# Performance work log

Hardware: AMD Instinct MI355X
Metric: run time of the kernel (lower is better)

## Reference

```python
import jax, jax.numpy as jnp
import numpy as np

B, S, D, A_DIM = 8, 2048, 256, 64

def setup_inputs() -> dict:
    key = jax.random.key(0)
    k_x, k_wm, k_wl, k_eps = jax.random.split(key, 4)
    return {
        "x": jax.random.normal(k_x, (B, S, D), dtype=jnp.float32),
        "W_mean": jax.random.normal(k_wm, (D, A_DIM), dtype=jnp.float32) * (1.0 / np.sqrt(D)),
        "b_mean": jnp.zeros((A_DIM,), dtype=jnp.float32),
        "W_logvar": jax.random.normal(k_wl, (D, A_DIM), dtype=jnp.float32) * (1.0 / np.sqrt(D)),
        "b_logvar": jnp.zeros((A_DIM,), dtype=jnp.float32),
        "eps": jax.random.normal(k_eps, (B, S, A_DIM), dtype=jnp.float32),
    }

def reference(x, W_mean, b_mean, W_logvar, b_logvar, eps):
    d = x.shape[-1]
    scale = 1.0 / jnp.sqrt(jnp.asarray(d, dtype=x.dtype))
    # S_det = x x^T / sqrt(d)  -> [B, S, S]
    scores = jnp.einsum("bsd,btd->bst", x, x) * scale
    attn = jax.nn.softmax(scores, axis=-1)
    # A_det = softmax(S) x  -> [B, S, D]
    A_det = jnp.einsum("bst,btd->bsd", attn, x)
    A_mean = A_det @ W_mean + b_mean        # [B, S, A_DIM]
    A_logvar = A_det @ W_logvar + b_logvar  # [B, S, A_DIM]
    A = A_mean + jnp.exp(0.5 * A_logvar) * eps  # sqrt(exp(logvar)) = exp(logvar/2)
    return (A_mean, A_logvar, A)
```

## Files before the change

kernel.cpp:

```cpp
#include <hip/hip_runtime.h>

#define B_ 8
#define S_ 2048
#define D_ 256

typedef _Float16 f16;
typedef f16 f16x2 __attribute__((ext_vector_type(2)));
typedef f16 f16x8 __attribute__((ext_vector_type(8)));
typedef float f32x16 __attribute__((ext_vector_type(16)));
typedef unsigned int u32;
typedef u32 u32x4 __attribute__((ext_vector_type(4)));

typedef const __attribute__((address_space(1))) unsigned int* gptr_t;
typedef __attribute__((address_space(3))) unsigned int* lptr_t;

__device__ __forceinline__ void gload_lds16(const void* g, void* l) {
  __builtin_amdgcn_global_load_lds((gptr_t)(unsigned long long)g,
                                   (lptr_t)(unsigned long long)l, 16, 0, 0);
}

__device__ __forceinline__ u32 packf16(float a, float b) {
  f16x2 t; t[0] = (f16)a; t[1] = (f16)b;
  return __builtin_bit_cast(u32, t);
}

__device__ __forceinline__ void barrier_raw() {
  __builtin_amdgcn_sched_barrier(0);
  __builtin_amdgcn_s_barrier();
  __builtin_amdgcn_sched_barrier(0);
}

__device__ __forceinline__ void pack16(const f32x16& p, int hi, u32x4& o0, u32x4& o1) {
#pragma unroll
  for (int c2 = 0; c2 < 2; ++c2) {
    u32 a1 = packf16(p[8 * c2 + 0], p[8 * c2 + 1]);
    u32 a2 = packf16(p[8 * c2 + 2], p[8 * c2 + 3]);
    u32 b1 = packf16(p[8 * c2 + 4], p[8 * c2 + 5]);
    u32 b2 = packf16(p[8 * c2 + 6], p[8 * c2 + 7]);
    u32 xa1 = __shfl_xor(a1, 32), xa2 = __shfl_xor(a2, 32);
    u32 xb1 = __shfl_xor(b1, 32), xb2 = __shfl_xor(b2, 32);
    u32x4 f;
    f[0] = hi ? xb1 : a1;
    f[1] = hi ? xb2 : a2;
    f[2] = hi ? b1 : xa1;
    f[3] = hi ? b2 : xa2;
    if (c2) o1 = f; else o0 = f;
  }
}

#define SC2F 0.09016844f
#define NMAXR 20.0f
#define SWZ(r, s) ((s) ^ ((r) & 3) ^ (((r) >> 2) & 3))

__global__ void prep(const float* __restrict__ x, const float* __restrict__ Wm,
                     const float* __restrict__ Wl, f16* __restrict__ xh,
                     f16* __restrict__ xt, float* __restrict__ n2,
                     f16* __restrict__ Wt) {
  __shared__ f16 tile[64][264];
  const int bid = blockIdx.x;
  const int t = threadIdx.x;
  if (bid < 256) {
    const int b = bid >> 5, st = bid & 31;
    const int s0 = st * 64;
    const float* xb = x + ((size_t)(b * S_ + s0)) * D_;
    f16* xhb = xh + ((size_t)(b * S_ + s0)) * D_;
#pragma unroll
    for (int it = 0; it < 16; ++it) {
      int flat = it * 256 + t;
      int r = flat >> 6, c4 = flat & 63;
      float4 v = *reinterpret_cast<const float4*>(xb + r * 256 + c4 * 4);
      f16 h0 = (f16)v.x, h1 = (f16)v.y, h2 = (f16)v.z, h3 = (f16)v.w;
      f16x2 p0 = {h0, h1}, p1 = {h2, h3};
      uint2 wv; wv.x = __builtin_bit_cast(u32, p0); wv.y = __builtin_bit_cast(u32, p1);
      *reinterpret_cast<uint2*>(xhb + r * 256 + c4 * 4) = wv;
      tile[r][c4 * 4 + 0] = h0; tile[r][c4 * 4 + 1] = h1;
      tile[r][c4 * 4 + 2] = h2; tile[r][c4 * 4 + 3] = h3;
    }
    __syncthreads();
    {
      int r = t >> 2, qd = t & 3;
      float s = 0.0f;
#pragma unroll
      for (int i = 0; i < 8; ++i) {
        f16x8 v = *reinterpret_cast<const f16x8*>(&tile[r][qd * 64 + i * 8]);
#pragma unroll
        for (int u = 0; u < 8; ++u) { float f = (float)v[u]; s += f * f; }
      }
      s += __shfl_xor(s, 1); s += __shfl_xor(s, 2);
      if (qd == 0) n2[b * S_ + s0 + r] = s;
    }
    {
      f16* xtb = xt + ((size_t)(b * D_ + t)) * S_ + s0;
#pragma unroll
      for (int s8 = 0; s8 < 8; ++s8) {
        f16x8 ov;
#pragma unroll
        for (int u = 0; u < 8; ++u) ov[u] = tile[s8 * 8 + u][t];
        *reinterpret_cast<f16x8*>(xtb + s8 * 8) = ov;
      }
    }
  } else {
    int idx = (bid - 256) * 1024 + t * 4;
    int j = idx >> 8, d = idx & 255;
#pragma unroll
    for (int k2 = 0; k2 < 4; ++k2) {
      float v = (j < 64) ? Wm[(d + k2) * 64 + j] : Wl[(d + k2) * 64 + (j - 64)];
      Wt[idx + k2] = (f16)v;
    }
  }
}

__launch_bounds__(512, 4)
__global__ void gemm1_kern(const f16* __restrict__ xh, const float* __restrict__ n2,
                           f16* __restrict__ P, float* __restrict__ Lp,
                           int b0, int bm, int bsh) {
  __shared__ f16 Aq[2][4096];
  __shared__ f16 Bk[2][8192];
  const int idx = blockIdx.x;
  const int bl = idx & bm;
  const int kt = (idx >> bsh) & 7;
  const int qt = idx >> (bsh + 3);
  const int b = b0 + bl;
  const int qb = qt * 128, kb = kt * 256;
  const int tid = threadIdx.x, lane = tid & 63, w = tid >> 6;
  const int l31 = lane & 31, hi = lane >> 5;
  const int wq = w >> 2, wk = w & 3;
  const f16* xb = xh + (size_t)b * S_ * D_;

#define G1_STAGE(st, pp)                                                       \
  {                                                                            \
    { int c = tid; int r = c >> 2, sl = c & 3; int cs = SWZ(r, sl);            \
      gload_lds16(xb + (size_t)(qb + r) * 256 + (st) * 32 + cs * 8,            \
                  &Aq[pp][0] + c * 8); }                                       \
    _Pragma("unroll") for (int i = 0; i < 2; ++i) {                            \
      int c = i * 512 + tid; int r = c >> 2, sl = c & 3; int cs = SWZ(r, sl);  \
      gload_lds16(xb + (size_t)(kb + r) * 256 + (st) * 32 + cs * 8,            \
                  &Bk[pp][0] + c * 8); }                                       \
  }

#define G1_COMP(pp)                                                           \
  { _Pragma("unroll") for (int kc = 0; kc < 2; ++kc) {                        \
      int s = kc * 2 + hi;                                                    \
      f16x8 af[2], bf[2];                                                     \
      _Pragma("unroll") for (int mi = 0; mi < 2; ++mi) {                      \
        int row = wk * 64 + mi * 32 + l31;                                    \
        af[mi] = *reinterpret_cast<const f16x8*>(&Bk[pp][row * 32 + SWZ(row, s) * 8]); } \
      _Pragma("unroll") for (int ni = 0; ni < 2; ++ni) {                      \
        int row = wq * 64 + ni * 32 + l31;                                    \
        bf[ni] = *reinterpret_cast<const f16x8*>(&Aq[pp][row * 32 + SWZ(row, s) * 8]); } \
      _Pragma("unroll") for (int mi = 0; mi < 2; ++mi)                        \
        _Pragma("unroll") for (int ni = 0; ni < 2; ++ni)                      \
          acc[mi][ni] = __builtin_amdgcn_mfma_f32_32x32x16_f16(af[mi], bf[ni], acc[mi][ni], 0, 0, 0); \
    } }

  f32x16 acc[2][2];
#pragma unroll
  for (int i = 0; i < 2; ++i)
#pragma unroll
    for (int j = 0; j < 2; ++j)
#pragma unroll
      for (int e = 0; e < 16; ++e) acc[i][j][e] = 0.0f;

  G1_STAGE(0, 0);
  __syncthreads();
#pragma unroll 1
  for (int t = 0; t < 8; ++t) {
    const int p = t & 1;
    if (t < 7) G1_STAGE(t + 1, p ^ 1);
    G1_COMP(p);
    __syncthreads();
  }
#undef G1_STAGE
#undef G1_COMP

  float r2[2], lsum[2];
  int qrow[2];
#pragma unroll
  for (int ni = 0; ni < 2; ++ni) {
    qrow[ni] = qb + wq * 64 + ni * 32 + l31;
    r2[ni] = sqrtf(n2[b * S_ + qrow[ni]]) * (NMAXR * SC2F);
    lsum[ni] = 0.0f;
  }
#pragma unroll
  for (int mi = 0; mi < 2; ++mi)
#pragma unroll
    for (int ni = 0; ni < 2; ++ni)
#pragma unroll
      for (int j = 0; j < 16; ++j) {
        float v = exp2f(acc[mi][ni][j] * SC2F - r2[ni]);
        acc[mi][ni][j] = v;
        lsum[ni] += v;
      }
#pragma unroll
  for (int ni = 0; ni < 2; ++ni) lsum[ni] += __shfl_xor(lsum[ni], 32);

#pragma unroll
  for (int mi = 0; mi < 2; ++mi)
#pragma unroll
    for (int ni = 0; ni < 2; ++ni) {
      u32x4 s0, s1;
      pack16(acc[mi][ni], hi, s0, s1);
      size_t rowp = (size_t)(bl * S_ + qrow[ni]) * 2048;
      int colb = kb + wk * 64 + mi * 32;
      *reinterpret_cast<u32x4*>(P + rowp + colb + hi * 8) = s0;
      *reinterpret_cast<u32x4*>(P + rowp + colb + 16 + hi * 8) = s1;
    }

  float* Lred = (float*)(&Aq[0][0]);
  if (hi == 0) {
    Lred[(wq * 64 + l31) * 4 + wk] = lsum[0];
    Lred[(wq * 64 + 32 + l31) * 4 + wk] = lsum[1];
  }
  __syncthreads();
  if (tid < 128) {
    float s = Lred[tid * 4] + Lred[tid * 4 + 1] + Lred[tid * 4 + 2] + Lred[tid * 4 + 3];
    Lp[(size_t)(bl * 8 + kt) * 2048 + qb + tid] = s;
  }
}

__launch_bounds__(256, 3)
__global__ void gemm2_kern(const f16* __restrict__ P, const f16* __restrict__ xt,
                           const float* __restrict__ Lp, f16* __restrict__ adet,
                           int b0, int bm, int bsh) {
  __shared__ f16 Pt[4][2048];
  __shared__ f16 Xt[4][4096];
  const int idx = blockIdx.x;
  const int bl = idx & bm;
  const int dt = (idx >> bsh) & 1;
  const int qt = idx >> (bsh + 1);
  const int b = b0 + bl;
  const int qb = qt * 64, db = dt * 128;
  const int tid = threadIdx.x, lane = tid & 63, w = tid >> 6;
  const int l31 = lane & 31, hi = lane >> 5;
  const int wq = w & 1, wd = w >> 1;
  const f16* xtb = xt + (size_t)b * D_ * S_;

#define G2_STAGE(tt, tb)                                                       \
  {                                                                            \
    { int c = tid; int r = c >> 2, sl = c & 3; int cs = SWZ(r, sl);            \
      gload_lds16(P + (size_t)(bl * S_ + qb + r) * 2048 + (tt) * 32 + cs * 8,  \
                  &Pt[tb][0] + c * 8); }                                       \
    _Pragma("unroll") for (int i = 0; i < 2; ++i) {                            \
      int c = i * 256 + tid; int r = c >> 2, sl = c & 3; int cs = SWZ(r, sl);  \
      gload_lds16(xtb + (size_t)(db + r) * 2048 + (tt) * 32 + cs * 8,          \
                  &Xt[tb][0] + c * 8); }                                       \
  }

#define G2_COMP(tb)                                                           \
  { _Pragma("unroll") for (int kc = 0; kc < 2; ++kc) {                        \
      int s = kc * 2 + hi;                                                    \
      int qrow = wq * 32 + l31;                                               \
      f16x8 bf = *reinterpret_cast<const f16x8*>(&Pt[tb][qrow * 32 + SWZ(qrow, s) * 8]); \
      _Pragma("unroll") for (int ni = 0; ni < 2; ++ni) {                      \
        int drow = wd * 64 + ni * 32 + l31;                                   \
        f16x8 af = *reinterpret_cast<const f16x8*>(&Xt[tb][drow * 32 + SWZ(drow, s) * 8]); \
        acc[ni] = __builtin_amdgcn_mfma_f32_32x32x16_f16(af, bf, acc[ni], 0, 0, 0); \
      } } }

  f32x16 acc[2];
#pragma unroll
  for (int i = 0; i < 2; ++i)
#pragma unroll
    for (int e = 0; e < 16; ++e) acc[i][e] = 0.0f;

  G2_STAGE(0, 0);
  G2_STAGE(1, 1);
  G2_STAGE(2, 2);
#pragma unroll 1
  for (int t = 0; t < 62; ++t) {
    asm volatile("s_waitcnt vmcnt(6)" ::: "memory");
    barrier_raw();
    if (t < 61) G2_STAGE(t + 3, (t + 3) & 3);
    G2_COMP(t & 3);
  }
  asm volatile("s_waitcnt vmcnt(3)" ::: "memory");
  barrier_raw();
  G2_COMP(2);
  asm volatile("s_waitcnt vmcnt(0)" ::: "memory");
  barrier_raw();
  G2_COMP(3);
#undef G2_STAGE
#undef G2_COMP

  const int q = qb + wq * 32 + l31;
  float L = 0.0f;
#pragma unroll
  for (int kt = 0; kt < 8; ++kt) L += Lp[(size_t)(bl * 8 + kt) * 2048 + q];
  float rL = 1.0f / L;
#pragma unroll
  for (int ni = 0; ni < 2; ++ni)
#pragma unroll
    for (int e = 0; e < 16; ++e) acc[ni][e] *= rL;
#pragma unroll
  for (int ni = 0; ni < 2; ++ni) {
    u32x4 s0, s1;
    pack16(acc[ni], hi, s0, s1);
    f16* arow = adet + (size_t)(b * S_ + q) * 256 + db + wd * 64 + ni * 32;
    *reinterpret_cast<u32x4*>(arow + hi * 8) = s0;
    *reinterpret_cast<u32x4*>(arow + 16 + hi * 8) = s1;
  }
}

__launch_bounds__(64)
__global__ void proj_kern(const f16* __restrict__ adet, const f16* __restrict__ Wt,
                          const float* __restrict__ bm, const float* __restrict__ bl,
                          const float* __restrict__ eps, float* __restrict__ out) {
  const int lane = threadIdx.x & 63;
  const int l31 = lane & 31, hi = lane >> 5;
  const int bidx = blockIdx.x;
  const int rb = ((bidx & 7) * 64 + (bidx >> 3)) * 32;
  f16x8 af[16];
  const f16* arow = adet + (size_t)(rb + l31) * 256;
#pragma unroll
  for (int kk = 0; kk < 16; ++kk)
    af[kk] = *reinterpret_cast<const f16x8*>(arow + kk * 16 + hi * 8);
  f32x16 acc[4];
#pragma unroll
  for (int i = 0; i < 4; ++i)
#pragma unroll
    for (int j = 0; j < 16; ++j) acc[i][j] = 0.0f;
#pragma unroll
  for (int ns = 0; ns < 4; ++ns) {
    const f16* wrow = Wt + (size_t)(l31 + 32 * ns) * 256;
#pragma unroll
    for (int kk = 0; kk < 16; ++kk) {
      f16x8 bf = *reinterpret_cast<const f16x8*>(wrow + kk * 16 + hi * 8);
      acc[ns] = __builtin_amdgcn_mfma_f32_32x32x16_f16(af[kk], bf, acc[ns], 0, 0, 0);
    }
  }
#pragma unroll
  for (int ns = 0; ns < 2; ++ns) {
    int c = l31 + 32 * ns;
    float bmv = bm[c], blv = bl[c];
#pragma unroll
    for (int r = 0; r < 16; ++r) {
      int row = (r & 3) + 8 * (r >> 2) + 4 * hi;
      int grow = rb + row;
      float mean = acc[ns][r] + bmv;
      float lv = acc[ns + 2][r] + blv;
      float e = eps[grow * 64 + c];
      float a = mean + exp2f(0.7213475204f * lv) * e;
      out[grow * 64 + c] = mean;
      out[1048576 + grow * 64 + c] = lv;
      out[2097152 + grow * 64 + c] = a;
    }
  }
}

extern "C" void kernel_launch(void* const* d_in, const int* in_sizes, int n_in,
                              void* d_out, int out_size, void* d_ws, size_t ws_size,
                              hipStream_t stream) {
  (void)in_sizes; (void)n_in; (void)out_size;
  const float* x   = (const float*)d_in[0];
  const float* Wm  = (const float*)d_in[1];
  const float* bmv = (const float*)d_in[2];
  const float* Wl  = (const float*)d_in[3];
  const float* blv = (const float*)d_in[4];
  const float* ep  = (const float*)d_in[5];
  float* out = (float*)d_out;

  char* ws = (char*)d_ws;
  f16*   xh   = (f16*)(ws + 0);
  f16*   xt   = (f16*)(ws + 8388608);
  f16*   adet = (f16*)(ws + 16777216);
  f16*   Wt   = (f16*)(ws + 25165824);
  float* n2   = (float*)(ws + 25231360);
  float* Lp   = (float*)(ws + 25296896);
  const size_t P_off = 25821184;
  f16*   Pbuf = (f16*)(ws + P_off);

  int bpp = 1;
  if      (ws_size >= P_off + (size_t)8 * 2048 * 2048 * 2) bpp = 8;
  else if (ws_size >= P_off + (size_t)4 * 2048 * 2048 * 2) bpp = 4;
  else if (ws_size >= P_off + (size_t)2 * 2048 * 2048 * 2) bpp = 2;
  const int bsh = (bpp == 8) ? 3 : (bpp == 4) ? 2 : (bpp == 2) ? 1 : 0;
  const int bm = bpp - 1;

  prep<<<288, 256, 0, stream>>>(x, Wm, Wl, xh, xt, n2, Wt);
  for (int b0 = 0; b0 < 8; b0 += bpp) {
    gemm1_kern<<<bpp * 128, 512, 0, stream>>>(xh, n2, Pbuf, Lp, b0, bm, bsh);
    gemm2_kern<<<bpp * 64, 256, 0, stream>>>(Pbuf, xt, Lp, adet, b0, bm, bsh);
  }
  proj_kern<<<512, 64, 0, stream>>>(adet, Wt, bmv, blv, ep, out);
}
```

Measured before the change: 89.81 us.

## Exploit score symmetry: compute upper-triangle tiles and mirror-write transposed P

Because scores = x x^T is symmetric, gemm1 now computes only the upper-triangular 128x128 tiles (136 per batch instead of the full grid) and writes both the tile and its transpose to P. The transposed tile is staged through shared memory with an XOR swizzle and exponentiated using the key-row norm bound. The row-sum partials buffer Lp is removed, and gemm2 instead accumulates the softmax denominator from the f16 P fragments it already loads. This halves the score GEMM FLOPs at the cost of an extra LDS transpose pass, a larger LDS footprint, and denominator sums taken from f16-rounded values.

```diff
diff --git a/kernel.cpp b/kernel.cpp
--- a/kernel.cpp
+++ b/kernel.cpp
@@ -112,116 +112,126 @@
 
 __launch_bounds__(512, 4)
 __global__ void gemm1_kern(const f16* __restrict__ xh, const float* __restrict__ n2,
-                           f16* __restrict__ P, float* __restrict__ Lp,
-                           int b0, int bm, int bsh) {
-  __shared__ f16 Aq[2][4096];
-  __shared__ f16 Bk[2][8192];
+                           f16* __restrict__ P, int b0, int bm, int bsh) {
+  __shared__ __align__(16) char smem[65536];
+  f16* Aq = (f16*)smem;
+  f16* Bk = (f16*)(smem + 32768);
   const int idx = blockIdx.x;
   const int bl = idx & bm;
-  const int kt = (idx >> bsh) & 7;
-  const int qt = idx >> (bsh + 3);
+  int tdec = idx >> bsh;
+  int qt = 0;
+#pragma unroll 1
+  while (tdec >= 16 - qt) { tdec -= 16 - qt; ++qt; }
+  const int kt = qt + tdec;
   const int b = b0 + bl;
-  const int qb = qt * 128, kb = kt * 256;
+  const int qb = qt * 128, kb = kt * 128;
   const int tid = threadIdx.x, lane = tid & 63, w = tid >> 6;
   const int l31 = lane & 31, hi = lane >> 5;
   const int wq = w >> 2, wk = w & 3;
   const f16* xb = xh + (size_t)b * S_ * D_;
 
 #define G1_STAGE(st, pp)                                                       \
-  {                                                                            \
-    { int c = tid; int r = c >> 2, sl = c & 3; int cs = SWZ(r, sl);            \
-      gload_lds16(xb + (size_t)(qb + r) * 256 + (st) * 32 + cs * 8,            \
-                  &Aq[pp][0] + c * 8); }                                       \
-    _Pragma("unroll") for (int i = 0; i < 2; ++i) {                            \
-      int c = i * 512 + tid; int r = c >> 2, sl = c & 3; int cs = SWZ(r, sl);  \
-      gload_lds16(xb + (size_t)(kb + r) * 256 + (st) * 32 + cs * 8,            \
-                  &Bk[pp][0] + c * 8); }                                       \
-  }
-
-#define G1_COMP(pp)                                                           \
-  { _Pragma("unroll") for (int kc = 0; kc < 2; ++kc) {                        \
-      int s = kc * 2 + hi;                                                    \
-      f16x8 af[2], bf[2];                                                     \
-      _Pragma("unroll") for (int mi = 0; mi < 2; ++mi) {                      \
-        int row = wk * 64 + mi * 32 + l31;                                    \
-        af[mi] = *reinterpret_cast<const f16x8*>(&Bk[pp][row * 32 + SWZ(row, s) * 8]); } \
-      _Pragma("unroll") for (int ni = 0; ni < 2; ++ni) {                      \
-        int row = wq * 64 + ni * 32 + l31;                                    \
-        bf[ni] = *reinterpret_cast<const f16x8*>(&Aq[pp][row * 32 + SWZ(row, s) * 8]); } \
-      _Pragma("unroll") for (int mi = 0; mi < 2; ++mi)                        \
-        _Pragma("unroll") for (int ni = 0; ni < 2; ++ni)                      \
-          acc[mi][ni] = __builtin_amdgcn_mfma_f32_32x32x16_f16(af[mi], bf[ni], acc[mi][ni], 0, 0, 0); \
+  { _Pragma("unroll") for (int i = 0; i < 4; ++i) {                            \
+      int ii = w * 4 + i;                                                      \
+      int flat = ii * 64 + lane;                                               \
+      bool isB = ii >= 16;                                                     \
+      int ch = isB ? flat - 1024 : flat;                                       \
+      int r = ch >> 3, c = ch & 7;                                             \
+      int csrc = c ^ (r & 7);                                                  \
+      const f16* src = xb + (size_t)((isB ? kb : qb) + r) * 256 +              \
+                       (st) * 64 + csrc * 8;                                   \
+      f16* dst = (isB ? Bk : Aq) + ((pp) * 8192) + ch * 8;                     \
+      gload_lds16(src, dst);                                                   \
     } }
 
-  f32x16 acc[2][2];
+  f32x16 acc[2];
 #pragma unroll
   for (int i = 0; i < 2; ++i)
 #pragma unroll
-    for (int j = 0; j < 2; ++j)
-#pragma unroll
-      for (int e = 0; e < 16; ++e) acc[i][j][e] = 0.0f;
+    for (int e = 0; e < 16; ++e) acc[i][e] = 0.0f;
 
   G1_STAGE(0, 0);
   __syncthreads();
-#pragma unroll 1
-  for (int t = 0; t < 8; ++t) {
+#pragma unroll
+  for (int t = 0; t < 4; ++t) {
     const int p = t & 1;
-    if (t < 7) G1_STAGE(t + 1, p ^ 1);
-    G1_COMP(p);
+    if (t < 3) G1_STAGE(t + 1, p ^ 1);
+#pragma unroll
+    for (int kc = 0; kc < 4; ++kc) {
+      int cc = ((2 * kc + hi) ^ (l31 & 7)) * 8;
+      f16x8 af  = *reinterpret_cast<const f16x8*>(Bk + p * 8192 + (wk * 32 + l31) * 64 + cc);
+      f16x8 bf0 = *reinterpret_cast<const f16x8*>(Aq + p * 8192 + (wq * 64 + l31) * 64 + cc);
+      f16x8 bf1 = *reinterpret_cast<const f16x8*>(Aq + p * 8192 + (wq * 64 + 32 + l31) * 64 + cc);
+      acc[0] = __builtin_amdgcn_mfma_f32_32x32x16_f16(af, bf0, acc[0], 0, 0, 0);
+      acc[1] = __builtin_amdgcn_mfma_f32_32x32x16_f16(af, bf1, acc[1], 0, 0, 0);
+    }
     __syncthreads();
   }
 #undef G1_STAGE
-#undef G1_COMP
-
-  float r2[2], lsum[2];
+
+  float* raw = (float*)smem;
+  if (kt != qt) {
+#pragma unroll
+    for (int ni = 0; ni < 2; ++ni)
+#pragma unroll
+      for (int j = 0; j < 16; ++j) {
+        int kvloc = wk * 32 + (j & 3) + 8 * (j >> 2) + 4 * hi;
+        int qloc = wq * 64 + ni * 32 + l31;
+        raw[kvloc * 128 + (qloc ^ ((kvloc & 7) << 2))] = acc[ni][j];
+      }
+  }
+
+  float r2[2];
   int qrow[2];
 #pragma unroll
   for (int ni = 0; ni < 2; ++ni) {
     qrow[ni] = qb + wq * 64 + ni * 32 + l31;
     r2[ni] = sqrtf(n2[b * S_ + qrow[ni]]) * (NMAXR * SC2F);
-    lsum[ni] = 0.0f;
-  }
-#pragma unroll
-  for (int mi = 0; mi < 2; ++mi)
-#pragma unroll
-    for (int ni = 0; ni < 2; ++ni)
-#pragma unroll
-      for (int j = 0; j < 16; ++j) {
-        float v = exp2f(acc[mi][ni][j] * SC2F - r2[ni]);
-        acc[mi][ni][j] = v;
-        lsum[ni] += v;
-      }
-#pragma unroll
-  for (int ni = 0; ni < 2; ++ni) lsum[ni] += __shfl_xor(lsum[ni], 32);
-
-#pragma unroll
-  for (int mi = 0; mi < 2; ++mi)
-#pragma unroll
-    for (int ni = 0; ni < 2; ++ni) {
-      u32x4 s0, s1;
-      pack16(acc[mi][ni], hi, s0, s1);
-      size_t rowp = (size_t)(bl * S_ + qrow[ni]) * 2048;
-      int colb = kb + wk * 64 + mi * 32;
-      *reinterpret_cast<u32x4*>(P + rowp + colb + hi * 8) = s0;
-      *reinterpret_cast<u32x4*>(P + rowp + colb + 16 + hi * 8) = s1;
-    }
-
-  float* Lred = (float*)(&Aq[0][0]);
-  if (hi == 0) {
-    Lred[(wq * 64 + l31) * 4 + wk] = lsum[0];
-    Lred[(wq * 64 + 32 + l31) * 4 + wk] = lsum[1];
-  }
-  __syncthreads();
-  if (tid < 128) {
-    float s = Lred[tid * 4] + Lred[tid * 4 + 1] + Lred[tid * 4 + 2] + Lred[tid * 4 + 3];
-    Lp[(size_t)(bl * 8 + kt) * 2048 + qb + tid] = s;
+  }
+#pragma unroll
+  for (int ni = 0; ni < 2; ++ni)
+#pragma unroll
+    for (int j = 0; j < 16; ++j)
+      acc[ni][j] = exp2f(acc[ni][j] * SC2F - r2[ni]);
+
+  const int colb = kb + wk * 32;
+#pragma unroll
+  for (int ni = 0; ni < 2; ++ni) {
+    u32x4 s0, s1;
+    pack16(acc[ni], hi, s0, s1);
+    size_t rowp = (size_t)(bl * S_ + qrow[ni]) * 2048;
+    *reinterpret_cast<u32x4*>(P + rowp + colb + hi * 8) = s0;
+    *reinterpret_cast<u32x4*>(P + rowp + colb + 16 + hi * 8) = s1;
+  }
+
+  if (kt != qt) {
+    __syncthreads();
+    const int kvr = tid >> 2;
+    const int qseg = (tid & 3) * 32;
+    float r2kv = sqrtf(n2[b * S_ + kb + kvr]) * (NMAXR * SC2F);
+    u32 ow[16];
+#pragma unroll
+    for (int c8 = 0; c8 < 8; ++c8) {
+      int qs = qseg + c8 * 4;
+      float4 v = *reinterpret_cast<const float4*>(
+          &raw[kvr * 128 + (qs ^ ((kvr & 7) << 2))]);
+      ow[c8 * 2 + 0] = packf16(exp2f(v.x * SC2F - r2kv), exp2f(v.y * SC2F - r2kv));
+      ow[c8 * 2 + 1] = packf16(exp2f(v.z * SC2F - r2kv), exp2f(v.w * SC2F - r2kv));
+    }
+    size_t rowp = (size_t)(bl * S_ + kb + kvr) * 2048;
+#pragma unroll
+    for (int sseg = 0; sseg < 4; ++sseg) {
+      u32x4 sv;
+      sv[0] = ow[sseg * 4 + 0]; sv[1] = ow[sseg * 4 + 1];
+      sv[2] = ow[sseg * 4 + 2]; sv[3] = ow[sseg * 4 + 3];
+      *reinterpret_cast<u32x4*>(P + rowp + qb + qseg + sseg * 8) = sv;
+    }
   }
 }
 
 __launch_bounds__(256, 3)
 __global__ void gemm2_kern(const f16* __restrict__ P, const f16* __restrict__ xt,
-                           const float* __restrict__ Lp, f16* __restrict__ adet,
-                           int b0, int bm, int bsh) {
+                           f16* __restrict__ adet, int b0, int bm, int bsh) {
   __shared__ f16 Pt[4][2048];
   __shared__ f16 Xt[4][4096];
   const int idx = blockIdx.x;
@@ -238,22 +248,27 @@
 #define G2_STAGE(tt, tb)                                                       \
   {                                                                            \
     { int c = tid; int r = c >> 2, sl = c & 3; int cs = SWZ(r, sl);            \
-      gload_lds16(P + (size_t)(bl * S_ + qb + r) * 2048 + (tt) * 32 + cs * 8,  \
-                  &Pt[tb][0] + c * 8); }                                       \
+      gload_lds16(P + (size_t)(bl * S_ + qb + r) * 2048 + ((tt) * 32) + cs * 8,\
+                  &Pt[(tb)][0] + c * 8); }                                     \
     _Pragma("unroll") for (int i = 0; i < 2; ++i) {                            \
       int c = i * 256 + tid; int r = c >> 2, sl = c & 3; int cs = SWZ(r, sl);  \
-      gload_lds16(xtb + (size_t)(db + r) * 2048 + (tt) * 32 + cs * 8,          \
-                  &Xt[tb][0] + c * 8); }                                       \
+      gload_lds16(xtb + (size_t)(db + r) * 2048 + ((tt) * 32) + cs * 8,        \
+                  &Xt[(tb)][0] + c * 8); }                                     \
   }
 
 #define G2_COMP(tb)                                                           \
   { _Pragma("unroll") for (int kc = 0; kc < 2; ++kc) {                        \
       int s = kc * 2 + hi;                                                    \
       int qrow = wq * 32 + l31;                                               \
-      f16x8 bf = *reinterpret_cast<const f16x8*>(&Pt[tb][qrow * 32 + SWZ(qrow, s) * 8]); \
+      f16x8 bf = *reinterpret_cast<const f16x8*>(&Pt[(tb)][qrow * 32 + SWZ(qrow, s) * 8]); \
+      { const f16x2* pp2 = reinterpret_cast<const f16x2*>(&bf);               \
+        f16x2 sa = pp2[0] + pp2[1];                                           \
+        f16x2 sb = pp2[2] + pp2[3];                                           \
+        sa = sa + sb;                                                         \
+        lsum += (float)sa[0] + (float)sa[1]; }                                \
       _Pragma("unroll") for (int ni = 0; ni < 2; ++ni) {                      \
         int drow = wd * 64 + ni * 32 + l31;                                   \
-        f16x8 af = *reinterpret_cast<const f16x8*>(&Xt[tb][drow * 32 + SWZ(drow, s) * 8]); \
+        f16x8 af = *reinterpret_cast<const f16x8*>(&Xt[(tb)][drow * 32 + SWZ(drow, s) * 8]); \
         acc[ni] = __builtin_amdgcn_mfma_f32_32x32x16_f16(af, bf, acc[ni], 0, 0, 0); \
       } } }
 
@@ -262,6 +277,7 @@
   for (int i = 0; i < 2; ++i)
 #pragma unroll
     for (int e = 0; e < 16; ++e) acc[i][e] = 0.0f;
+  float lsum = 0.0f;
 
   G2_STAGE(0, 0);
   G2_STAGE(1, 1);
@@ -283,9 +299,7 @@
 #undef G2_COMP
 
   const int q = qb + wq * 32 + l31;
-  float L = 0.0f;
-#pragma unroll
-  for (int kt = 0; kt < 8; ++kt) L += Lp[(size_t)(bl * 8 + kt) * 2048 + q];
+  float L = lsum + __shfl_xor(lsum, 32);
   float rL = 1.0f / L;
 #pragma unroll
   for (int ni = 0; ni < 2; ++ni)
@@ -365,7 +379,6 @@
   f16*   adet = (f16*)(ws + 16777216);
   f16*   Wt   = (f16*)(ws + 25165824);
   float* n2   = (float*)(ws + 25231360);
-  float* Lp   = (float*)(ws + 25296896);
   const size_t P_off = 25821184;
   f16*   Pbuf = (f16*)(ws + P_off);
 
@@ -378,8 +391,8 @@
 
   prep<<<288, 256, 0, stream>>>(x, Wm, Wl, xh, xt, n2, Wt);
   for (int b0 = 0; b0 < 8; b0 += bpp) {
-    gemm1_kern<<<bpp * 128, 512, 0, stream>>>(xh, n2, Pbuf, Lp, b0, bm, bsh);
-    gemm2_kern<<<bpp * 64, 256, 0, stream>>>(Pbuf, xt, Lp, adet, b0, bm, bsh);
+    gemm1_kern<<<bpp * 136, 512, 0, stream>>>(xh, n2, Pbuf, b0, bm, bsh);
+    gemm2_kern<<<bpp * 64, 256, 0, stream>>>(Pbuf, xt, adet, b0, bm, bsh);
   }
   proj_kern<<<512, 64, 0, stream>>>(adet, Wt, bmv, blv, ep, out);
 }
```

New measurement: 89.51 us. Within noise of the previous version (-0.3%).
